# Kernel optimization log

Hardware: AMD Instinct MI355X
Metric: run time of the kernel (lower is better)

The kernel has to match this reference:

```python
import jax, jax.numpy as jnp
import numpy as np

L_CLASS, L_NOOBJ, L_OBJ, L_BOX = 2.0, 1.0, 5.0, 10.0


def _bce_with_logits(x, t):
    # -t*log(sigmoid(x)) - (1-t)*log(1-sigmoid(x)) = softplus(x) - t*x  (stable)
    return jax.nn.softplus(x) - t * x


def _iou_midpoint(a, b, eps=1e-6):
    # a, b: [..., 4] boxes in (cx, cy, w, h) format
    ax1, ay1 = a[..., 0] - a[..., 2] / 2, a[..., 1] - a[..., 3] / 2
    ax2, ay2 = a[..., 0] + a[..., 2] / 2, a[..., 1] + a[..., 3] / 2
    bx1, by1 = b[..., 0] - b[..., 2] / 2, b[..., 1] - b[..., 3] / 2
    bx2, by2 = b[..., 0] + b[..., 2] / 2, b[..., 1] + b[..., 3] / 2
    iw = jnp.clip(jnp.minimum(ax2, bx2) - jnp.maximum(ax1, bx1), 0.0)
    ih = jnp.clip(jnp.minimum(ay2, by2) - jnp.maximum(ay1, by1), 0.0)
    inter = iw * ih
    area_a = jnp.abs((ax2 - ax1) * (ay2 - ay1))
    area_b = jnp.abs((bx2 - bx1) * (by2 - by1))
    return inter / (area_a + area_b - inter + eps)


def setup_inputs() -> dict:
    key = jax.random.key(0)
    k1, k2, k3, k4, k5 = jax.random.split(key, 5)
    B, A, S, C = 32, 3, 52, 80
    predictions = jax.random.normal(k1, (B, A, S, S, 5 + C), dtype=jnp.float32) * 0.5
    obj = (jax.random.uniform(k2, (B, A, S, S)) < 0.05).astype(jnp.float32)
    xy = jax.random.uniform(k3, (B, A, S, S, 2), dtype=jnp.float32)          # cell offsets in (0,1)
    wh = jax.random.uniform(k4, (B, A, S, S, 2), dtype=jnp.float32, minval=0.5, maxval=10.0)
    cls = jax.random.randint(k5, (B, A, S, S), 0, C).astype(jnp.float32)
    targets = jnp.concatenate([obj[..., None], xy, wh, cls[..., None]], axis=-1)
    # YOLOv3 anchors for the S=52 scale, in grid-cell units
    anchor = jnp.array([[1.25, 1.625], [2.0, 3.75], [4.125, 2.875]], dtype=jnp.float32)
    return {"predictions": predictions, "targets": targets, "anchor": anchor}


def reference(predictions, targets, anchor):
    t0 = targets[..., 0]                       # [B,A,S,S] objectness
    obj = t0 == 1.0
    noobj = t0 == 0.0
    n_obj = jnp.maximum(jnp.sum(obj.astype(jnp.float32)), 1.0)
    n_noobj = jnp.maximum(jnp.sum(noobj.astype(jnp.float32)), 1.0)

    # no-object loss: BCEWithLogits on raw objectness logit, mean over noobj cells
    no_object_loss = jnp.sum(jnp.where(noobj, _bce_with_logits(predictions[..., 0], t0), 0.0)) / n_noobj

    anc = anchor.reshape(1, 3, 1, 1, 2)
    pxy = jax.nn.sigmoid(predictions[..., 1:3])
    pwh = jnp.exp(predictions[..., 3:5]) * anc
    box_preds = jnp.concatenate([pxy, pwh], axis=-1)

    # IoU on detached decoded boxes vs target boxes
    ious = _iou_midpoint(jax.lax.stop_gradient(box_preds), targets[..., 1:5])  # [B,A,S,S]

    # object loss: note original applies sigmoid, then BCEWithLogits (double squash) -- kept faithful
    sp = jax.nn.sigmoid(predictions[..., 0])
    object_loss = jnp.sum(jnp.where(obj, _bce_with_logits(sp, ious * t0), 0.0)) / n_obj

    # box loss: MSE between [sigmoid(xy), raw wh logits] and [target xy, log(wh/anchor)]
    twh = jnp.log(1e-16 + targets[..., 3:5] / anc)
    tbox = jnp.concatenate([targets[..., 1:3], twh], axis=-1)
    pbox = jnp.concatenate([pxy, predictions[..., 3:5]], axis=-1)
    box_loss = jnp.sum(jnp.where(obj[..., None], (pbox - tbox) ** 2, 0.0)) / (4.0 * n_obj)

    # class loss: cross-entropy over obj cells
    logp = jax.nn.log_softmax(predictions[..., 5:], axis=-1)
    cls_idx = targets[..., 5].astype(jnp.int32)
    ce = -jnp.take_along_axis(logp, cls_idx[..., None], axis=-1)[..., 0]
    class_loss = jnp.sum(jnp.where(obj, ce, 0.0)) / n_obj

    return (L_BOX * box_loss + L_OBJ * object_loss
            + L_NOOBJ * no_object_loss + L_CLASS * class_loss)
```

## Files before the change

kernel.cpp:

```cpp
#include <hip/hip_runtime.h>
#include <math.h>

#define CPG (52 * 52)
#define PSTRIDE 2048
#define MAXOBJ 64

__device__ __forceinline__ float softplusf(float x) {
    if (x > 20.f)  return x;
    if (x < -20.f) return expf(x);
    return log1pf(expf(x));
}
__device__ __forceinline__ float sigmoidf(float x) {
    return 1.f / (1.f + expf(-x));
}

__global__ __launch_bounds__(256) void yolo_main_kernel(
    const float* __restrict__ pred,
    const float* __restrict__ targ,
    const float* __restrict__ anchor,
    float* __restrict__ part,
    int n_cells)
{
    __shared__ int   s_cnt;
    __shared__ int   s_list[MAXOBJ];
    __shared__ float red[6][4];

    const int tid = threadIdx.x;
    const int idx = blockIdx.x * 256 + tid;

    if (tid == 0) s_cnt = 0;
    __syncthreads();

    const bool v = (idx < n_cells);
    float t0 = v ? targ[(size_t)idx * 6]  : -1.f;
    float x0 = v ? pred[(size_t)idx * 85] : 0.f;

    float noobj_s = 0.f, nobj_c = 0.f, nnoobj_c = 0.f;

    if (t0 == 0.0f) {
        noobj_s = softplusf(x0);
        nnoobj_c = 1.f;
    } else if (t0 == 1.0f) {
        nobj_c = 1.f;
        int pos = atomicAdd(&s_cnt, 1);
        if (pos < MAXOBJ) s_list[pos] = idx;
    }

    __syncthreads();

    float box_s = 0.f, obj_s = 0.f, cls_s = 0.f;
    {
        const int n   = min(s_cnt, MAXOBJ);
        const int grp = tid >> 5;
        const int k   = tid & 31;
        for (int c = grp; c < n; c += 8) {
            const int cell = s_list[c];
            const float* __restrict__ p = pred + (size_t)cell * 85;

            float e = expf(p[5 + k]) + expf(p[37 + k]);
            if (k < 16) e += expf(p[69 + k]);
            #pragma unroll
            for (int off = 1; off < 32; off <<= 1)
                e += __shfl_xor(e, off, 32);

            if (k == 0) {
                const float2* __restrict__ t2 = (const float2*)(targ + (size_t)cell * 6);
                float2 ta = t2[0], tb = t2[1], tc = t2[2];
                const float px0 = p[0], l1 = p[1], l2 = p[2], rw = p[3], rh = p[4];

                const int a = (cell / CPG) % 3;
                const float aw = anchor[a * 2 + 0];
                const float ah = anchor[a * 2 + 1];

                const float tx = ta.y, ty = tb.x, tw = tb.y, th = tc.x;
                const int   ci = (int)tc.y;

                const float px = sigmoidf(l1);
                const float py = sigmoidf(l2);
                const float pw = expf(rw) * aw;
                const float ph = expf(rh) * ah;

                float ax1 = px - pw * 0.5f, ay1 = py - ph * 0.5f;
                float ax2 = px + pw * 0.5f, ay2 = py + ph * 0.5f;
                float bx1 = tx - tw * 0.5f, by1 = ty - th * 0.5f;
                float bx2 = tx + tw * 0.5f, by2 = ty + th * 0.5f;
                float iw = fmaxf(fminf(ax2, bx2) - fmaxf(ax1, bx1), 0.f);
                float ih = fmaxf(fminf(ay2, by2) - fmaxf(ay1, by1), 0.f);
                float inter  = iw * ih;
                float area_a = fabsf((ax2 - ax1) * (ay2 - ay1));
                float area_b = fabsf((bx2 - bx1) * (by2 - by1));
                float iou = inter / (area_a + area_b - inter + 1e-6f);

                float sp = sigmoidf(px0);
                obj_s += softplusf(sp) - iou * sp;

                float twx = logf(1e-16f + tw / aw);
                float twy = logf(1e-16f + th / ah);
                float d1 = px - tx, d2 = py - ty, d3 = rw - twx, d4 = rh - twy;
                box_s += d1 * d1 + d2 * d2 + d3 * d3 + d4 * d4;

                cls_s += logf(e) - p[5 + ci];
            }
        }
    }

    float sums[6] = {box_s, obj_s, noobj_s, cls_s, nobj_c, nnoobj_c};
    #pragma unroll
    for (int k = 0; k < 6; ++k) {
        float vv = sums[k];
        #pragma unroll
        for (int off = 32; off > 0; off >>= 1)
            vv += __shfl_down(vv, off, 64);
        sums[k] = vv;
    }

    const int lane = tid & 63;
    const int wave = tid >> 6;
    if (lane == 0) {
        #pragma unroll
        for (int k = 0; k < 6; ++k) red[k][wave] = sums[k];
    }
    __syncthreads();

    if (tid < 6) {
        int k = tid;
        part[k * PSTRIDE + blockIdx.x] =
            (red[k][0] + red[k][1]) + (red[k][2] + red[k][3]);
    }
}

__global__ __launch_bounds__(256) void yolo_finalize_kernel(
    const float* __restrict__ part,
    float* __restrict__ out,
    int n_blocks)
{
    const int tid  = threadIdx.x;
    const int lane = tid & 63;
    const int wave = tid >> 6;

    float s[6];
    #pragma unroll
    for (int k = 0; k < 6; ++k) {
        float v = 0.f;
        for (int i = tid; i < n_blocks; i += 256)
            v += part[k * PSTRIDE + i];
        #pragma unroll
        for (int off = 32; off > 0; off >>= 1)
            v += __shfl_down(v, off, 64);
        s[k] = v;
    }

    __shared__ float red[6][4];
    if (lane == 0) {
        #pragma unroll
        for (int k = 0; k < 6; ++k) red[k][wave] = s[k];
    }
    __syncthreads();

    if (tid == 0) {
        float a[6];
        #pragma unroll
        for (int k = 0; k < 6; ++k)
            a[k] = (red[k][0] + red[k][1]) + (red[k][2] + red[k][3]);
        float n_o  = fmaxf(a[4], 1.f);
        float n_no = fmaxf(a[5], 1.f);
        out[0] = 10.f * a[0] / (4.f * n_o)
               + 5.f  * a[1] / n_o
               + 1.f  * a[2] / n_no
               + 2.f  * a[3] / n_o;
    }
}

extern "C" void kernel_launch(void* const* d_in, const int* in_sizes, int n_in,
                              void* d_out, int out_size, void* d_ws, size_t ws_size,
                              hipStream_t stream) {
    const float* pred   = (const float*)d_in[0];
    const float* targ   = (const float*)d_in[1];
    const float* anchor = (const float*)d_in[2];
    float* part = (float*)d_ws;
    float* out  = (float*)d_out;

    int n_cells = in_sizes[1] / 6;
    int blocks  = (n_cells + 255) / 256;

    yolo_main_kernel<<<blocks, 256, 0, stream>>>(pred, targ, anchor, part, n_cells);
    yolo_finalize_kernel<<<1, 256, 0, stream>>>(part, out, blocks);
}
```

Measured before the change: 140.4 us.

## Split no-object loss into a coalesced float4 streaming kernel over predictions

Takes the per-cell no-object softplus out of the main kernel, which loaded the objectness logit with an 85-float stride per thread. A new grid-stride kernel reads the whole prediction tensor as coalesced float4 vectors with four loads in flight per thread. From each vector's flat index it works out whether it holds a cell's element 0, reads that cell's target, and adds softplus for no-object cells into a separate partial slot. This swaps scattered one-float-per-line reads for full-bandwidth streaming, at the price of reading every prediction byte plus an extra kernel launch and reshuffled finalize indices.

Measured after the change: 161.3 us. 1.15x slower.

```diff
diff --git a/kernel.cpp b/kernel.cpp
--- a/kernel.cpp
+++ b/kernel.cpp
@@ -4,6 +4,7 @@
 #define CPG (52 * 52)
 #define PSTRIDE 2048
 #define MAXOBJ 64
+#define K2_BLOCKS 2048
 
 __device__ __forceinline__ float softplusf(float x) {
     if (x > 20.f)  return x;
@@ -14,7 +15,8 @@
     return 1.f / (1.f + expf(-x));
 }
 
-__global__ __launch_bounds__(256) void yolo_main_kernel(
+
+__global__ __launch_bounds__(256) void k1_targets(
     const float* __restrict__ pred,
     const float* __restrict__ targ,
     const float* __restrict__ anchor,
@@ -23,7 +25,7 @@
 {
     __shared__ int   s_cnt;
     __shared__ int   s_list[MAXOBJ];
-    __shared__ float red[6][4];
+    __shared__ float red[5][4];
 
     const int tid = threadIdx.x;
     const int idx = blockIdx.x * 256 + tid;
@@ -32,20 +34,16 @@
     __syncthreads();
 
     const bool v = (idx < n_cells);
-    float t0 = v ? targ[(size_t)idx * 6]  : -1.f;
-    float x0 = v ? pred[(size_t)idx * 85] : 0.f;
-
-    float noobj_s = 0.f, nobj_c = 0.f, nnoobj_c = 0.f;
-
+    float t0 = v ? targ[(size_t)idx * 6] : -1.f;
+
+    float nobj_c = 0.f, nnoobj_c = 0.f;
     if (t0 == 0.0f) {
-        noobj_s = softplusf(x0);
         nnoobj_c = 1.f;
     } else if (t0 == 1.0f) {
         nobj_c = 1.f;
         int pos = atomicAdd(&s_cnt, 1);
         if (pos < MAXOBJ) s_list[pos] = idx;
     }
-
     __syncthreads();
 
     float box_s = 0.f, obj_s = 0.f, cls_s = 0.f;
@@ -66,7 +64,7 @@
             if (k == 0) {
                 const float2* __restrict__ t2 = (const float2*)(targ + (size_t)cell * 6);
                 float2 ta = t2[0], tb = t2[1], tc = t2[2];
-                const float px0 = p[0], l1 = p[1], l2 = p[2], rw = p[3], rh = p[4];
+                const float x0 = p[0], l1 = p[1], l2 = p[2], rw = p[3], rh = p[4];
 
                 const int a = (cell / CPG) % 3;
                 const float aw = anchor[a * 2 + 0];
@@ -91,7 +89,7 @@
                 float area_b = fabsf((bx2 - bx1) * (by2 - by1));
                 float iou = inter / (area_a + area_b - inter + 1e-6f);
 
-                float sp = sigmoidf(px0);
+                float sp = sigmoidf(x0);
                 obj_s += softplusf(sp) - iou * sp;
 
                 float twx = logf(1e-16f + tw / aw);
@@ -104,35 +102,85 @@
         }
     }
 
-    float sums[6] = {box_s, obj_s, noobj_s, cls_s, nobj_c, nnoobj_c};
+    float sums[5] = {box_s, obj_s, cls_s, nobj_c, nnoobj_c};
     #pragma unroll
-    for (int k = 0; k < 6; ++k) {
+    for (int k = 0; k < 5; ++k) {
         float vv = sums[k];
         #pragma unroll
         for (int off = 32; off > 0; off >>= 1)
             vv += __shfl_down(vv, off, 64);
         sums[k] = vv;
     }
-
     const int lane = tid & 63;
     const int wave = tid >> 6;
     if (lane == 0) {
         #pragma unroll
-        for (int k = 0; k < 6; ++k) red[k][wave] = sums[k];
-    }
-    __syncthreads();
-
-    if (tid < 6) {
-        int k = tid;
-        part[k * PSTRIDE + blockIdx.x] =
-            (red[k][0] + red[k][1]) + (red[k][2] + red[k][3]);
-    }
+        for (int k = 0; k < 5; ++k) red[k][wave] = sums[k];
+    }
+    __syncthreads();
+    if (tid < 5)
+        part[tid * PSTRIDE + blockIdx.x] =
+            (red[tid][0] + red[tid][1]) + (red[tid][2] + red[tid][3]);
+}
+
+__device__ __forceinline__ float k2_contrib(
+    float4 x, long long i, const float* __restrict__ targ)
+{
+    unsigned f   = (unsigned)(i << 2);
+    unsigned c   = f / 85u;
+    unsigned rem = f - c * 85u;
+    int      j;
+    unsigned cell;
+    bool     has;
+    if (rem == 0u) { has = true; j = 0; cell = c; }
+    else           { j = 85 - (int)rem; has = (j <= 3); cell = c + 1u; }
+    if (!has) return 0.f;
+    float t0 = targ[(size_t)cell * 6];
+    if (t0 != 0.0f) return 0.f;
+    float v = (j == 0) ? x.x : (j == 1) ? x.y : (j == 2) ? x.z : x.w;
+    return softplusf(v);
+}
+
+__global__ __launch_bounds__(256) void k2_stream(
+    const float4* __restrict__ p4,
+    const float* __restrict__ targ,
+    float* __restrict__ part,
+    long long n4)
+{
+    const long long stride = (long long)K2_BLOCKS * 256;
+    long long i = (long long)blockIdx.x * 256 + threadIdx.x;
+
+    float s0 = 0.f, s1 = 0.f, s2 = 0.f, s3 = 0.f;
+    for (; i + 3 * stride < n4; i += 4 * stride) {
+        float4 a = p4[i];
+        float4 b = p4[i + stride];
+        float4 c = p4[i + 2 * stride];
+        float4 d = p4[i + 3 * stride];
+        s0 += k2_contrib(a, i, targ);
+        s1 += k2_contrib(b, i + stride, targ);
+        s2 += k2_contrib(c, i + 2 * stride, targ);
+        s3 += k2_contrib(d, i + 3 * stride, targ);
+    }
+    for (; i < n4; i += stride) s0 += k2_contrib(p4[i], i, targ);
+
+    float s = (s0 + s1) + (s2 + s3);
+    #pragma unroll
+    for (int off = 32; off > 0; off >>= 1)
+        s += __shfl_down(s, off, 64);
+
+    __shared__ float red[4];
+    const int lane = threadIdx.x & 63;
+    const int wv   = threadIdx.x >> 6;
+    if (lane == 0) red[wv] = s;
+    __syncthreads();
+    if (threadIdx.x == 0)
+        part[5 * PSTRIDE + blockIdx.x] = (red[0] + red[1]) + (red[2] + red[3]);
 }
 
 __global__ __launch_bounds__(256) void yolo_finalize_kernel(
     const float* __restrict__ part,
     float* __restrict__ out,
-    int n_blocks)
+    int n1)
 {
     const int tid  = threadIdx.x;
     const int lane = tid & 63;
@@ -141,8 +189,9 @@
     float s[6];
     #pragma unroll
     for (int k = 0; k < 6; ++k) {
+        int lim = (k < 5) ? n1 : K2_BLOCKS;
         float v = 0.f;
-        for (int i = tid; i < n_blocks; i += 256)
+        for (int i = tid; i < lim; i += 256)
             v += part[k * PSTRIDE + i];
         #pragma unroll
         for (int off = 32; off > 0; off >>= 1)
@@ -162,12 +211,12 @@
         #pragma unroll
         for (int k = 0; k < 6; ++k)
             a[k] = (red[k][0] + red[k][1]) + (red[k][2] + red[k][3]);
-        float n_o  = fmaxf(a[4], 1.f);
-        float n_no = fmaxf(a[5], 1.f);
+        float n_o  = fmaxf(a[3], 1.f);
+        float n_no = fmaxf(a[4], 1.f);
         out[0] = 10.f * a[0] / (4.f * n_o)
                + 5.f  * a[1] / n_o
-               + 1.f  * a[2] / n_no
-               + 2.f  * a[3] / n_o;
+               + 1.f  * a[5] / n_no
+               + 2.f  * a[2] / n_o;
     }
 }
 
@@ -180,9 +229,11 @@
     float* part = (float*)d_ws;
     float* out  = (float*)d_out;
 
-    int n_cells = in_sizes[1] / 6;
-    int blocks  = (n_cells + 255) / 256;
-
-    yolo_main_kernel<<<blocks, 256, 0, stream>>>(pred, targ, anchor, part, n_cells);
-    yolo_finalize_kernel<<<1, 256, 0, stream>>>(part, out, blocks);
-}
+    const int n_cells = in_sizes[1] / 6;
+    const long long n4 = (long long)in_sizes[0] / 4;
+    const int n1 = (n_cells + 255) / 256;
+
+    k1_targets<<<n1, 256, 0, stream>>>(pred, targ, anchor, part, n_cells);
+    k2_stream<<<K2_BLOCKS, 256, 0, stream>>>((const float4*)pred, targ, part, n4);
+    yolo_finalize_kernel<<<1, 256, 0, stream>>>(part, out, n1);
+}
```
